# Kernel tuning notes

Measured on AMD Instinct MI355X. Metric: run time of the kernel, lower is better.

Reference implementation:

```python
import jax, jax.numpy as jnp
import numpy as np

B, T, N = 2048, 500, 64
DT = 0.25  # integration step
V_TH = 30.0

# Izhikevich behaviour params: (a, b, c, d, v0); u0 = b * v0
LLBN_P = (0.02, 0.20, -65.0, 6.0, -70.0)   # LLBN_behaviour (tonic-spiking-like)
EBN_P  = (0.02, 0.25, -55.0, 0.05, -64.0)  # phasic bursting
IFN_P  = (0.02, 0.25, -65.0, 6.0, -64.0)   # phasic spiking
TN_P   = (0.02, 0.20, -50.0, 2.0, -70.0)   # tonic bursting
MN_P   = IFN_P                              # phasic spiking


def izh_step(v, u, I, p):
    """One Euler step of the Izhikevich neuron; returns (spike, v_new, u_new)."""
    a, b, c, d, _ = p
    v_ = v + DT * (0.04 * v * v + 5.0 * v + 140.0 - u + I)
    u_ = u + DT * a * (b * v - u)
    z = (v_ >= V_TH).astype(v.dtype)
    v_new = jnp.where(z > 0, c, v_)
    u_new = u_ + z * d
    return z, v_new, u_new


def init_state(p, batch):
    a, b, c, d, v0 = p
    return jnp.full((batch,), v0, jnp.float32), jnp.full((batch,), b * v0, jnp.float32)


def setup_inputs() -> dict:
    key = jax.random.key(0)
    k1, k2 = jax.random.split(key)
    input_mat = jax.random.uniform(k1, (B, T, N), dtype=jnp.float32)
    weights_matrix = jax.random.uniform(k2, (24,), dtype=jnp.float32)
    return {"input_mat": input_mat, "weights_matrix": weights_matrix}


def _run(input_mat, w):
    # summed retinal drive per timestep; [B, T] -> [T, B] for scan
    zp1 = (input_mat * w[0]).sum(-1).T
    zp2 = (input_mat * w[12]).sum(-1).T

    vL, uL = init_state(LLBN_P, B); zL = jnp.zeros((B,), jnp.float32)
    vE, uE = init_state(EBN_P, B)
    vI, uI = init_state(IFN_P, B)
    vT, uT = init_state(TN_P, B); zT = jnp.zeros((B,), jnp.float32)
    vM, uM = init_state(MN_P, B)
    # channel 2 uses the SAME cells (self.LLBN/EBN/... are reused in the
    # original forward, so weights w[2],w[3],w[9],w[10] apply) with its own state
    vL2, uL2 = vL, uL; zL2 = zL
    vE2, uE2 = vE, uE
    vI2, uI2 = vI, uI
    vT2, uT2 = vT, uT; zT2 = zT
    vM2, uM2 = vM, uM

    carry0 = (vL, uL, zL, vE, uE, vI, uI, vT, uT, zT, vM, uM,
              vL2, uL2, zL2, vE2, uE2, vI2, uI2, vT2, uT2, zT2, vM2, uM2)

    def step(carry, zin):
        (vL, uL, zL, vE, uE, vI, uI, vT, uT, zT, vM, uM,
         vL2, uL2, zL2, vE2, uE2, vI2, uI2, vT2, uT2, zT2, vM2, uM2) = carry
        zp, zp2 = zin
        # --- channel 1 ---  (temp feedback is always 0 in the original: local var)
        z2, vL, uL = izh_step(vL, uL, w[2] * (zp * w[1]) + w[3] * zL, LLBN_P)
        z3, vE, uE = izh_step(vE, uE, zp * w[4] + z2 * w[5], EBN_P)
        z4, vI, uI = izh_step(vI, uI, z3 * w[6], IFN_P)
        z5, vT, uT = izh_step(vT, uT, w[9] * (z3 * w[8]) + w[10] * zT, TN_P)
        z6, vM, uM = izh_step(vM, uM, z5 * w[11], MN_P)
        # --- channel 2 ---
        z22, vL2, uL2 = izh_step(vL2, uL2, w[2] * (zp2 * w[13]) + w[3] * zL2, LLBN_P)
        z32, vE2, uE2 = izh_step(vE2, uE2, zp2 * w[16] + z22 * w[17], EBN_P)
        z42, vI2, uI2 = izh_step(vI2, uI2, z32 * w[18], IFN_P)
        z52, vT2, uT2 = izh_step(vT2, uT2, w[9] * (z32 * w[20]) + w[10] * zT2, TN_P)
        z62, vM2, uM2 = izh_step(vM2, uM2, z52 * w[23], MN_P)
        new_carry = (vL, uL, z2, vE, uE, vI, uI, vT, uT, z5, vM, uM,
                     vL2, uL2, z22, vE2, uE2, vI2, uI2, vT2, uT2, z52, vM2, uM2)
        outs = (z6, vM, z62, vM2,
                jnp.stack([z2, z3, z4, z5], -1),   # o_spikes_o [B,4]
                jnp.stack([vL, vE, vI, vT], -1))   # v_o        [B,4]
        return new_carry, outs

    _, (o_spikes, v, o_spikes2, v2, o_spikes_o, v_o) = jax.lax.scan(step, carry0, (zp1, zp2))
    # scan stacks on leading T axis -> move to [B, T, ...]
    tr = lambda a: jnp.moveaxis(a, 0, 1)
    return tr(o_spikes), tr(v), tr(o_spikes2), tr(v2), tr(o_spikes_o), tr(v_o)


def reference(input_mat, weights_matrix):
    return _run(input_mat, weights_matrix)
```

## Files before the change

kernel.cpp:

```cpp
#include <hip/hip_runtime.h>

#define B_ 2048
#define T_ 500
#define BT (B_ * T_)

__device__ __forceinline__ float izh_m(float& v, float& u, float I,
                                       float b, float c, float d, bool valid) {
    float t  = 0.04f * v * v + 5.0f * v + 140.0f - u + I;
    float v_ = v + 0.25f * t;
    float u_ = u + 0.005f * (b * v - u);
    float z  = (v_ >= 30.0f) ? 1.0f : 0.0f;
    float vn = (v_ >= 30.0f) ? c : v_;
    float un = u_ + z * d;
    if (!valid) { z = 0.f; vn = v; un = u; }
    v = vn; u = un;
    return z;
}

__device__ __forceinline__ float dpp_shr1(float x) {
    return __int_as_float(__builtin_amdgcn_update_dpp(
        0, __float_as_int(x), 0x111, 0xf, 0xf, true));
}

#define BAR() do {                                                             \
    asm volatile("s_waitcnt lgkmcnt(0)" ::: "memory");                         \
    __builtin_amdgcn_s_barrier();                                              \
    __builtin_amdgcn_sched_barrier(0);                                         \
} while (0)

__global__ __launch_bounds__(128) void fused_scan10_kernel(
        const float* __restrict__ in, const float* __restrict__ w24,
        float* __restrict__ out) {
    __shared__ float S_lds[128];
    __shared__ float ring[64 * 56];

    const int tid   = threadIdx.x;
    const int wid   = tid >> 6;
    const int lane  = tid & 63;
    const int bbase = blockIdx.x << 2;

    const int c     = lane >> 4;
    const int slot  = lane & 15;
    const int chl   = slot >> 3;
    const int role8 = slot & 7;

    const float a0   = chl ? w24[12] : w24[0];
    const float W1v  = chl ? w24[13] : w24[1];
    const float W4v  = chl ? w24[16] : w24[4];
    const float W5x  = chl ? w24[17] : w24[5];
    const float W6v  = chl ? w24[18] : w24[6];
    const float W8v  = chl ? w24[20] : w24[8];
    const float W11v = chl ? w24[23] : w24[11];
    const float W2 = w24[2], W3 = w24[3], W9 = w24[9], W10 = w24[10];

    float pb, pcc, pd, v, u, wA, wB, wC, wD;
    float fL = 0.f, fE = 0.f, fITM = 0.f;
    int offs;
    if (role8 == 0 || role8 == 4) {
        pb=0.20f; pcc=-65.f; pd=6.f;   v=-70.f; u=-14.f;
        wA=W2;  wB=W1v;  wC=0.f; wD=W3;  offs=0; fL=1.f;
    } else if (role8 == 1 || role8 == 5) {
        pb=0.25f; pcc=-55.f; pd=0.05f; v=-64.f; u=-16.f;
        wA=1.f; wB=W4v;  wC=W5x; wD=0.f; offs=3; fE=1.f;
    } else if (role8 == 2) {
        pb=0.25f; pcc=-65.f; pd=6.f;   v=-64.f; u=-16.f;
        wA=1.f; wB=W6v;  wC=0.f; wD=0.f; offs=6; fITM=1.f;
    } else if (role8 == 6) {
        pb=0.20f; pcc=-50.f; pd=2.f;   v=-70.f; u=-14.f;
        wA=W9;  wB=W8v;  wC=0.f; wD=W10; offs=6; fITM=1.f;
    } else if (role8 == 7) {
        pb=0.25f; pcc=-65.f; pd=6.f;   v=-64.f; u=-16.f;
        wA=1.f; wB=W11v; wC=0.f; wD=0.f; offs=9; fITM=1.f;
    } else {
        pb=0.25f; pcc=-65.f; pd=6.f;   v=-64.f; u=-16.f;
        wA=0.f; wB=0.f;  wC=0.f; wD=0.f; offs=9;
    }
    const bool wr = (chl == 0 && (role8 <= 2 || role8 == 6 || role8 == 7))
                 || (chl == 1 && role8 == 7);
    int p = 0;
    if (role8 == 1) p = 1;
    else if (role8 == 2) p = 2;
    else if (role8 == 6) p = 3;
    else if (role8 == 7) p = chl ? 5 : 4;
    const int ringoff = c * 14 + 2 * p;

    float z_last = 0.f, in_p1 = 0.f, in_p2 = 0.f;
    float zp1 = 0.f, zp2 = 0.f, zp3 = 0.f;

    const int lr = lane >> 4, ltt = lane & 15;
    const float* inb = in + (size_t)bbase * T_ * 64;
    float4 A[16], Bv[16];

#define ISSUE(KK, BUF) {                                                       \
    const int t0i = 16 * (KK);                                                 \
    const int ttc = (t0i + ltt <= 499) ? ltt : 0;                              \
    const float* ap = inb + ((size_t)lr * T_ + t0i + ttc) * 64;                \
    _Pragma("unroll")                                                          \
    for (int ck = 0; ck < 16; ++ck) BUF[ck] = *(const float4*)(ap + ck * 4);   \
}

#define REDUCE(KK, BUF) {                                                      \
    float* sw = S_lds + ((KK) & 1) * 64;                                       \
    float q0,q1,q2,q3,q4,q5,q6,q7,q8,q9,q10,q11,q12,q13,q14,q15;               \
    { float4 t_;                                                               \
      t_=BUF[0];  q0 =(t_.x+t_.y)+(t_.z+t_.w);                                 \
      t_=BUF[1];  q1 =(t_.x+t_.y)+(t_.z+t_.w);                                 \
      t_=BUF[2];  q2 =(t_.x+t_.y)+(t_.z+t_.w);                                 \
      t_=BUF[3];  q3 =(t_.x+t_.y)+(t_.z+t_.w);                                 \
      t_=BUF[4];  q4 =(t_.x+t_.y)+(t_.z+t_.w);                                 \
      t_=BUF[5];  q5 =(t_.x+t_.y)+(t_.z+t_.w);                                 \
      t_=BUF[6];  q6 =(t_.x+t_.y)+(t_.z+t_.w);                                 \
      t_=BUF[7];  q7 =(t_.x+t_.y)+(t_.z+t_.w);                                 \
      t_=BUF[8];  q8 =(t_.x+t_.y)+(t_.z+t_.w);                                 \
      t_=BUF[9];  q9 =(t_.x+t_.y)+(t_.z+t_.w);                                 \
      t_=BUF[10]; q10=(t_.x+t_.y)+(t_.z+t_.w);                                 \
      t_=BUF[11]; q11=(t_.x+t_.y)+(t_.z+t_.w);                                 \
      t_=BUF[12]; q12=(t_.x+t_.y)+(t_.z+t_.w);                                 \
      t_=BUF[13]; q13=(t_.x+t_.y)+(t_.z+t_.w);                                 \
      t_=BUF[14]; q14=(t_.x+t_.y)+(t_.z+t_.w);                                 \
      t_=BUF[15]; q15=(t_.x+t_.y)+(t_.z+t_.w); }                               \
    float a0_=q0+q1, a1_=q2+q3, a2_=q4+q5, a3_=q6+q7;                          \
    float a4_=q8+q9, a5_=q10+q11, a6_=q12+q13, a7_=q14+q15;                    \
    float b0_=a0_+a1_, b1_=a2_+a3_, b2_=a4_+a5_, b3_=a6_+a7_;                  \
    float c0_=b0_+b1_, c1_=b2_+b3_;                                            \
    float s_ = c0_ + c1_;                                                      \
    sw[lr * 16 + ltt] = (16 * (KK) + ltt <= 499) ? s_ : 0.f;                   \
}

#define SYS_ITER(SV, VEXPR, I_) {                                              \
    float in0 = in_p2;                                                         \
    in_p2 = in_p1;                                                             \
    in_p1 = dpp_shr1(z_last);                                                  \
    float zpc = (SV) * a0;                                                     \
    float X = (fL * zpc + fE * zp3) + fITM * in0;                              \
    float Isyn = wA * (X * wB) + wC * in0 + wD * z_last;                       \
    float znew = izh_m(v, u, Isyn, pb, pcc, pd, (VEXPR));                      \
    if (wr) *(float2*)(ringp + (I_) * 56) = make_float2(znew, v);              \
    zp3 = zp2; zp2 = zp1; zp1 = zpc;                                           \
    z_last = znew;                                                             \
}

#define GROUP16(VF)                                                            \
    SYS_ITER(g0.x, VF(0),  0)  SYS_ITER(g0.y, VF(1),  1)                       \
    SYS_ITER(g0.z, VF(2),  2)  SYS_ITER(g0.w, VF(3),  3)                       \
    SYS_ITER(g1.x, VF(4),  4)  SYS_ITER(g1.y, VF(5),  5)                       \
    SYS_ITER(g1.z, VF(6),  6)  SYS_ITER(g1.w, VF(7),  7)                       \
    SYS_ITER(g2.x, VF(8),  8)  SYS_ITER(g2.y, VF(9),  9)                       \
    SYS_ITER(g2.z, VF(10), 10) SYS_ITER(g2.w, VF(11), 11)                      \
    SYS_ITER(g3.x, VF(12), 12) SYS_ITER(g3.y, VF(13), 13)                      \
    SYS_ITER(g3.z, VF(14), 14) SYS_ITER(g3.w, VF(15), 15)

#define VF_PRO(i)  ((i) >= offs)
#define VF_ONE(i)  true
#define VF_EPI(i)  ((i) <= 3 + offs)

#define DUMP(K) {                                                              \
    const int td = lane & 15;                                                  \
    const int cc = lane >> 4;                                                  \
    const int t  = 16 * (K) - 9 + td;                                          \
    if (0 <= t && t <= 499) {                                                  \
        const float* rb = ring + cc * 14;                                      \
        float2 a2 = *(const float2*)&rb[((t)     & 63) * 56 + 0];              \
        float2 b2 = *(const float2*)&rb[((t + 3) & 63) * 56 + 2];              \
        float2 c1 = *(const float2*)&rb[((t + 6) & 63) * 56 + 4];              \
        float2 c2 = *(const float2*)&rb[((t + 6) & 63) * 56 + 6];              \
        float2 e1 = *(const float2*)&rb[((t + 9) & 63) * 56 + 8];              \
        float2 e2 = *(const float2*)&rb[((t + 9) & 63) * 56 + 10];             \
        const size_t g = (size_t)(bbase + cc) * T_ + t;                        \
        out[g]          = e1.x;                           \
        out[BT + g]     = e1.y;                           \
        out[2 * BT + g] = e2.x;                           \
        out[3 * BT + g] = e2.y;                           \
        ((float4*)out)[BT + g]     = make_float4(a2.x, b2.x, c1.x, c2.x);      \
        ((float4*)out)[2 * BT + g] = make_float4(a2.y, b2.y, c1.y, c2.y);      \
    }                                                                          \
}

#define SCANP(K, VFSEL) {                                                      \
    const float4* sp = (const float4*)(S_lds + ((K) & 1) * 64 + c * 16);       \
    float4 g0 = sp[0], g1 = sp[1], g2 = sp[2], g3 = sp[3];                     \
    float* ringp = ring + ((K) & 3) * 896 + ringoff;                           \
    __builtin_amdgcn_s_setprio(1);                                             \
    GROUP16(VFSEL)                                                             \
    __builtin_amdgcn_s_setprio(0);                                             \
}

    if (wid == 1) {
        ISSUE(0, A)
        REDUCE(0, A)
        ISSUE(1, Bv)
    }
    BAR();

    for (int k = 0; k < 32; k += 2) {
        if (wid == 0) {
            if (k == 0) { SCANP(k, VF_PRO) } else { SCANP(k, VF_ONE) }
        } else {
            if (k + 2 < 32) { ISSUE(k + 2, A) }
            if (k + 1 < 32) { REDUCE(k + 1, Bv) }
            if (k >= 1) { DUMP(k - 1) }
        }
        BAR();
        if (wid == 0) {
            if (k + 1 == 31) { SCANP(k + 1, VF_EPI) } else { SCANP(k + 1, VF_ONE) }
        } else {
            if (k + 3 < 32) { ISSUE(k + 3, Bv) }
            if (k + 2 < 32) { REDUCE(k + 2, A) }
            DUMP(k)
        }
        BAR();
    }
    if (wid == 1) { DUMP(31) }

#undef ISSUE
#undef REDUCE
#undef SYS_ITER
#undef GROUP16
#undef VF_PRO
#undef VF_ONE
#undef VF_EPI
#undef DUMP
#undef SCANP
}

extern "C" void kernel_launch(void* const* d_in, const int* in_sizes, int n_in,
                              void* d_out, int out_size, void* d_ws, size_t ws_size,
                              hipStream_t stream) {
    const float* in = (const float*)d_in[0];
    const float* w  = (const float*)d_in[1];
    float* out = (float*)d_out;

    fused_scan10_kernel<<<512, 128, 0, stream>>>(in, w, out);
}
```

Measured before the change: 74.59 us.

## Map one batch row per block and reduce input rows with quad DPP

Each block now handles a single batch row instead of four, giving four times as many blocks. The loader wave splits each timestep's 64 floats across four lanes and combines the partial sums with quad-permute DPP adds, cutting per-lane buffers from 16 to 4 float4s. The LDS ring shrinks to one row, and the scan-priority hints are removed. The scan wave still runs all four 16-lane groups, but only group 0 stores results, so three quarters of the scan lanes do discarded work. The aim is more concurrent waves and loads in flight to hide memory and serial-chain latency.

```diff
diff --git a/kernel.cpp b/kernel.cpp
--- a/kernel.cpp
+++ b/kernel.cpp
@@ -21,6 +21,14 @@
     return __int_as_float(__builtin_amdgcn_update_dpp(
         0, __float_as_int(x), 0x111, 0xf, 0xf, true));
 }
+__device__ __forceinline__ float dpp_qx1(float x) {
+    return __int_as_float(__builtin_amdgcn_update_dpp(
+        0, __float_as_int(x), 0xB1, 0xf, 0xf, true));
+}
+__device__ __forceinline__ float dpp_qx2(float x) {
+    return __int_as_float(__builtin_amdgcn_update_dpp(
+        0, __float_as_int(x), 0x4E, 0xf, 0xf, true));
+}
 
 #define BAR() do {                                                             \
     asm volatile("s_waitcnt lgkmcnt(0)" ::: "memory");                         \
@@ -28,16 +36,16 @@
     __builtin_amdgcn_sched_barrier(0);                                         \
 } while (0)
 
-__global__ __launch_bounds__(128) void fused_scan10_kernel(
+__global__ __launch_bounds__(128, 4) void fused_scan11_kernel(
         const float* __restrict__ in, const float* __restrict__ w24,
         float* __restrict__ out) {
     __shared__ float S_lds[128];
-    __shared__ float ring[64 * 56];
+    __shared__ float ring[64 * 14];
 
     const int tid   = threadIdx.x;
     const int wid   = tid >> 6;
     const int lane  = tid & 63;
-    const int bbase = blockIdx.x << 2;
+    const int b     = blockIdx.x;
 
     const int c     = lane >> 4;
     const int slot  = lane & 15;
@@ -75,56 +83,44 @@
         pb=0.25f; pcc=-65.f; pd=6.f;   v=-64.f; u=-16.f;
         wA=0.f; wB=0.f;  wC=0.f; wD=0.f; offs=9;
     }
-    const bool wr = (chl == 0 && (role8 <= 2 || role8 == 6 || role8 == 7))
-                 || (chl == 1 && role8 == 7);
+    const bool wr = (c == 0) &&
+        ((chl == 0 && (role8 <= 2 || role8 == 6 || role8 == 7)) ||
+         (chl == 1 && role8 == 7));
     int p = 0;
     if (role8 == 1) p = 1;
     else if (role8 == 2) p = 2;
     else if (role8 == 6) p = 3;
     else if (role8 == 7) p = chl ? 5 : 4;
-    const int ringoff = c * 14 + 2 * p;
+    const int ringoff = 2 * p;
 
     float z_last = 0.f, in_p1 = 0.f, in_p2 = 0.f;
     float zp1 = 0.f, zp2 = 0.f, zp3 = 0.f;
 
-    const int lr = lane >> 4, ltt = lane & 15;
-    const float* inb = in + (size_t)bbase * T_ * 64;
-    float4 A[16], Bv[16];
+    const int latom = lane >> 2, lchunk = lane & 3;
+    const float* inb = in + (size_t)b * T_ * 64;
+    float4 A[4], Bv[4];
 
 #define ISSUE(KK, BUF) {                                                       \
     const int t0i = 16 * (KK);                                                 \
-    const int ttc = (t0i + ltt <= 499) ? ltt : 0;                              \
-    const float* ap = inb + ((size_t)lr * T_ + t0i + ttc) * 64;                \
+    const int ttc = (t0i + latom <= 499) ? latom : 0;                          \
+    const float* ap = inb + (size_t)(t0i + ttc) * 64 + lchunk * 16;            \
     _Pragma("unroll")                                                          \
-    for (int ck = 0; ck < 16; ++ck) BUF[ck] = *(const float4*)(ap + ck * 4);   \
+    for (int ck = 0; ck < 4; ++ck) BUF[ck] = *(const float4*)(ap + ck * 4);    \
 }
 
 #define REDUCE(KK, BUF) {                                                      \
-    float* sw = S_lds + ((KK) & 1) * 64;                                       \
-    float q0,q1,q2,q3,q4,q5,q6,q7,q8,q9,q10,q11,q12,q13,q14,q15;               \
-    { float4 t_;                                                               \
-      t_=BUF[0];  q0 =(t_.x+t_.y)+(t_.z+t_.w);                                 \
-      t_=BUF[1];  q1 =(t_.x+t_.y)+(t_.z+t_.w);                                 \
-      t_=BUF[2];  q2 =(t_.x+t_.y)+(t_.z+t_.w);                                 \
-      t_=BUF[3];  q3 =(t_.x+t_.y)+(t_.z+t_.w);                                 \
-      t_=BUF[4];  q4 =(t_.x+t_.y)+(t_.z+t_.w);                                 \
-      t_=BUF[5];  q5 =(t_.x+t_.y)+(t_.z+t_.w);                                 \
-      t_=BUF[6];  q6 =(t_.x+t_.y)+(t_.z+t_.w);                                 \
-      t_=BUF[7];  q7 =(t_.x+t_.y)+(t_.z+t_.w);                                 \
-      t_=BUF[8];  q8 =(t_.x+t_.y)+(t_.z+t_.w);                                 \
-      t_=BUF[9];  q9 =(t_.x+t_.y)+(t_.z+t_.w);                                 \
-      t_=BUF[10]; q10=(t_.x+t_.y)+(t_.z+t_.w);                                 \
-      t_=BUF[11]; q11=(t_.x+t_.y)+(t_.z+t_.w);                                 \
-      t_=BUF[12]; q12=(t_.x+t_.y)+(t_.z+t_.w);                                 \
-      t_=BUF[13]; q13=(t_.x+t_.y)+(t_.z+t_.w);                                 \
-      t_=BUF[14]; q14=(t_.x+t_.y)+(t_.z+t_.w);                                 \
-      t_=BUF[15]; q15=(t_.x+t_.y)+(t_.z+t_.w); }                               \
-    float a0_=q0+q1, a1_=q2+q3, a2_=q4+q5, a3_=q6+q7;                          \
-    float a4_=q8+q9, a5_=q10+q11, a6_=q12+q13, a7_=q14+q15;                    \
-    float b0_=a0_+a1_, b1_=a2_+a3_, b2_=a4_+a5_, b3_=a6_+a7_;                  \
-    float c0_=b0_+b1_, c1_=b2_+b3_;                                            \
-    float s_ = c0_ + c1_;                                                      \
-    sw[lr * 16 + ltt] = (16 * (KK) + ltt <= 499) ? s_ : 0.f;                   \
+    float4 t_;                                                                 \
+    t_ = BUF[0]; float q0_ = (t_.x + t_.y) + (t_.z + t_.w);                    \
+    t_ = BUF[1]; float q1_ = (t_.x + t_.y) + (t_.z + t_.w);                    \
+    t_ = BUF[2]; float q2_ = (t_.x + t_.y) + (t_.z + t_.w);                    \
+    t_ = BUF[3]; float q3_ = (t_.x + t_.y) + (t_.z + t_.w);                    \
+    float a0_ = q0_ + q1_, a1_ = q2_ + q3_;                                    \
+    float bs_ = a0_ + a1_;                                                     \
+    float cs_ = bs_ + dpp_qx1(bs_);                                            \
+    float ss_ = cs_ + dpp_qx2(cs_);                                            \
+    if (lchunk == 0)                                                           \
+        S_lds[((KK) & 1) * 64 + latom] =                                       \
+            (16 * (KK) + latom <= 499) ? ss_ : 0.f;                            \
 }
 
 #define SYS_ITER(SV, VEXPR, I_) {                                              \
@@ -135,7 +131,7 @@
     float X = (fL * zpc + fE * zp3) + fITM * in0;                              \
     float Isyn = wA * (X * wB) + wC * in0 + wD * z_last;                       \
     float znew = izh_m(v, u, Isyn, pb, pcc, pd, (VEXPR));                      \
-    if (wr) *(float2*)(ringp + (I_) * 56) = make_float2(znew, v);              \
+    if (wr) *(float2*)(ringp + (I_) * 14) = make_float2(znew, v);              \
     zp3 = zp2; zp2 = zp1; zp1 = zpc;                                           \
     z_last = znew;                                                             \
 }
@@ -156,17 +152,15 @@
 
 #define DUMP(K) {                                                              \
     const int td = lane & 15;                                                  \
-    const int cc = lane >> 4;                                                  \
     const int t  = 16 * (K) - 9 + td;                                          \
-    if (0 <= t && t <= 499) {                                                  \
-        const float* rb = ring + cc * 14;                                      \
-        float2 a2 = *(const float2*)&rb[((t)     & 63) * 56 + 0];              \
-        float2 b2 = *(const float2*)&rb[((t + 3) & 63) * 56 + 2];              \
-        float2 c1 = *(const float2*)&rb[((t + 6) & 63) * 56 + 4];              \
-        float2 c2 = *(const float2*)&rb[((t + 6) & 63) * 56 + 6];              \
-        float2 e1 = *(const float2*)&rb[((t + 9) & 63) * 56 + 8];              \
-        float2 e2 = *(const float2*)&rb[((t + 9) & 63) * 56 + 10];             \
-        const size_t g = (size_t)(bbase + cc) * T_ + t;                        \
+    if (lane < 16 && 0 <= t && t <= 499) {                                     \
+        float2 a2 = *(const float2*)&ring[((t)     & 63) * 14 + 0];            \
+        float2 b2 = *(const float2*)&ring[((t + 3) & 63) * 14 + 2];            \
+        float2 c1 = *(const float2*)&ring[((t + 6) & 63) * 14 + 4];            \
+        float2 c2 = *(const float2*)&ring[((t + 6) & 63) * 14 + 6];            \
+        float2 e1 = *(const float2*)&ring[((t + 9) & 63) * 14 + 8];            \
+        float2 e2 = *(const float2*)&ring[((t + 9) & 63) * 14 + 10];           \
+        const size_t g = (size_t)b * T_ + t;                                   \
         out[g]          = e1.x;                           \
         out[BT + g]     = e1.y;                           \
         out[2 * BT + g] = e2.x;                           \
@@ -179,10 +173,8 @@
 #define SCANP(K, VFSEL) {                                                      \
     const float4* sp = (const float4*)(S_lds + ((K) & 1) * 64 + c * 16);       \
     float4 g0 = sp[0], g1 = sp[1], g2 = sp[2], g3 = sp[3];                     \
-    float* ringp = ring + ((K) & 3) * 896 + ringoff;                           \
-    __builtin_amdgcn_s_setprio(1);                                             \
+    float* ringp = ring + ((K) & 3) * 224 + ringoff;                           \
     GROUP16(VFSEL)                                                             \
-    __builtin_amdgcn_s_setprio(0);                                             \
 }
 
     if (wid == 1) {
@@ -230,5 +222,5 @@
     const float* w  = (const float*)d_in[1];
     float* out = (float*)d_out;
 
-    fused_scan10_kernel<<<512, 128, 0, stream>>>(in, w, out);
-}
+    fused_scan11_kernel<<<B_, 128, 0, stream>>>(in, w, out);
+}
```

Result: faster. 69.36 us (median of 2 runs) (-7.0%).
